# Optimization experiments

Hardware: AMD Instinct MI355X
Metric: run time of the kernel (lower is better)

## Reference

```python
import jax, jax.numpy as jnp
import numpy as np

B, T, P, D = 8, 2048, 4, 768

def setup_inputs() -> dict:
    key = jax.random.key(0)
    k1, k2, k3 = jax.random.split(key, 3)
    text_inputs = jax.random.normal(k1, (B, T, D), dtype=jnp.float32)
    sit_mask = jax.random.randint(k2, (B, T), 0, 2).astype(jnp.float32)
    proposition_matrix = jax.random.normal(k3, (B, T, P, D), dtype=jnp.float32)
    return {"text_inputs": text_inputs, "sit_mask": sit_mask, "proposition_matrix": proposition_matrix}

def reference(text_inputs, sit_mask, proposition_matrix):
    # D from proposition_matrix (matches text hidden dim), used for softmax scaling
    d = proposition_matrix.shape[-1]
    t = text_inputs.shape[1]
    # raw scores [B,T,T], scaled by 1/sqrt(D)
    scores = jnp.einsum('bid,bjd->bij', text_inputs, text_inputs) * (1.0 / jnp.sqrt(jnp.asarray(d, text_inputs.dtype)))
    # causal mask: strictly upper triangular -> -inf (tokens attend to self + past)
    causal = jnp.tril(jnp.ones((t, t), dtype=bool))  # [T,T]
    scores = jnp.where(causal[None, :, :], scores, -jnp.inf)
    weights = jax.nn.softmax(scores, axis=2)
    # padding mask via outer product of sit_mask; zero AFTER softmax (no renorm), as in original
    pad = (sit_mask[:, :, None] * sit_mask[:, None, :]) != 0  # [B,T,T]
    weights = jnp.where(pad, weights, jnp.zeros((), weights.dtype))
    out = jnp.einsum('bij,bjd->bid', weights, text_inputs)  # [B,T,D]
    # concat_self_hidden=True
    out = jnp.concatenate([out, text_inputs], axis=-1)  # [B,T,2D]
    return out
```

## Files before the change

kernel.cpp:

```cpp
#include <hip/hip_runtime.h>
#include <math.h>

constexpr int kT = 2048;
constexpr int kD = 768;

typedef __attribute__((ext_vector_type(8))) short short8;
typedef __attribute__((ext_vector_type(4))) float f32x4;
typedef __attribute__((ext_vector_type(16))) float f32x16;

#define FB(f) __builtin_bit_cast(unsigned, (f))
__device__ __forceinline__ unsigned pk_hi16(unsigned hi, unsigned lo) {
  return __builtin_amdgcn_perm(hi, lo, 0x07060302);
}
__device__ __forceinline__ unsigned pk_lo16(unsigned hi, unsigned lo) {
  return __builtin_amdgcn_perm(hi, lo, 0x05040100);
}

__device__ __forceinline__ void lds_barrier() {
  asm volatile("" ::: "memory");
  __builtin_amdgcn_s_waitcnt(0xC07F);
  __builtin_amdgcn_s_barrier();
  asm volatile("" ::: "memory");
}

__global__ __launch_bounds__(256, 2) void attn_mfma3(
    const float* __restrict__ x, const float* __restrict__ mask,
    float* __restrict__ out)
{
  const int tid = threadIdx.x;
  const int w = tid >> 6, l = tid & 63;
  const int l15 = l & 15, q4 = l >> 4;
  const int l31 = l & 31, h2 = l >> 5;

  const int bid = (int)blockIdx.x;
  const int b  = bid & 7;
  const int i0 = (63 - (bid >> 3)) << 5;

  const float* xb = x + (size_t)b * kT * kD;
  const float* mrow = mask + (size_t)b * kT;

  __shared__ unsigned short xK[16][776];
  __shared__ unsigned short VTb[192 * 64];
  __shared__ float sPart[4][16][36];
  __shared__ unsigned short Pm[32][16];
  __shared__ float corrS[32];
  __shared__ float invlS[32];

  short8 qf[2][6];
#pragma unroll
  for (int mt = 0; mt < 2; ++mt) {
    const int row = i0 + 16 * mt + l15;
#pragma unroll
    for (int s = 0; s < 6; ++s) {
      const float* p = xb + (size_t)row * kD + 192 * w + 32 * s + 8 * q4;
      float4 f0 = *(const float4*)p;
      float4 f1 = *(const float4*)(p + 4);
      uint4 u;
      u.x = pk_hi16(FB(f0.y), FB(f0.x));
      u.y = pk_hi16(FB(f0.w), FB(f0.z));
      u.z = pk_hi16(FB(f1.y), FB(f1.x));
      u.w = pk_hi16(FB(f1.w), FB(f1.z));
      qf[mt][s] = __builtin_bit_cast(short8, u);
    }
  }

  f32x16 o[6];
#pragma unroll
  for (int nt = 0; nt < 6; ++nt)
#pragma unroll
    for (int e = 0; e < 16; ++e) o[nt][e] = 0.0f;

  float mrun = -INFINITY, lrun = 0.0f;
  const float scale = 0.036084391824351615f;
  const int nTiles = i0 / 16 + 2;

  const int q = tid & 7, sr = tid >> 3;
  const int jA = (q >> 1) + 8 * (q & 1);
  const int irow = i0 + sr;

  const int D0 = 48 * w + (l31 >> 2);
  const int vtb_off0 = D0 * 64 + (((l31 & 3) ^ (D0 & 3)) << 4)
                     + ((8 * h2) ^ (8 * ((l31 >> 4) & 1)));

  float4 pf[3][4];
#pragma unroll
  for (int it = 0; it < 3; ++it)
#pragma unroll
    for (int jj = 0; jj < 4; ++jj)
      pf[it][jj] = *(const float4*)(xb + (size_t)(q4 + 4 * jj) * kD
                                    + 4 * (l15 + 16 * it + 48 * w));

  for (int t = 0; t < nTiles; ++t) {
    const int j0 = t * 16;
    const float mskA = mrow[j0 + jA];
    const float mskB = mrow[j0 + jA + 4];

    lds_barrier();

#pragma unroll
    for (int it = 0; it < 3; ++it) {
      const int d4 = l15 + 16 * it + 48 * w;
      unsigned lo[4], hi[4];
#pragma unroll
      for (int jj = 0; jj < 4; ++jj) {
        lo[jj] = pk_hi16(FB(pf[it][jj].y), FB(pf[it][jj].x));
        hi[jj] = pk_hi16(FB(pf[it][jj].w), FB(pf[it][jj].z));
      }
#pragma unroll
      for (int jj = 0; jj < 4; ++jj) {
        uint2 v; v.x = lo[jj]; v.y = hi[jj];
        *(uint2*)&xK[q4 + 4 * jj][4 * d4] = v;
      }
      const int D = d4;
      const int jb = (4 * q4) ^ (8 * ((D >> 2) & 1));
      const int base = D * 64 + jb;
      uint2 v;
      v.x = pk_lo16(lo[1], lo[0]); v.y = pk_lo16(lo[3], lo[2]);
      *(uint2*)&VTb[base + (((0 ^ (D & 3))) << 4)] = v;
      v.x = pk_hi16(lo[1], lo[0]); v.y = pk_hi16(lo[3], lo[2]);
      *(uint2*)&VTb[base + (((1 ^ (D & 3))) << 4)] = v;
      v.x = pk_lo16(hi[1], hi[0]); v.y = pk_lo16(hi[3], hi[2]);
      *(uint2*)&VTb[base + (((2 ^ (D & 3))) << 4)] = v;
      v.x = pk_hi16(hi[1], hi[0]); v.y = pk_hi16(hi[3], hi[2]);
      *(uint2*)&VTb[base + (((3 ^ (D & 3))) << 4)] = v;
    }

    if (t + 1 < nTiles) {
      const int jn = j0 + 16;
#pragma unroll
      for (int it = 0; it < 3; ++it)
#pragma unroll
        for (int jj = 0; jj < 4; ++jj)
          pf[it][jj] = *(const float4*)(xb + (size_t)(jn + q4 + 4 * jj) * kD
                                        + 4 * (l15 + 16 * it + 48 * w));
    }
    lds_barrier();

    {
      f32x4 sf0, sf1;
#pragma unroll
      for (int e = 0; e < 4; ++e) { sf0[e] = 0.f; sf1[e] = 0.f; }
#pragma unroll
      for (int s = 0; s < 6; ++s) {
        short8 kb = *(const short8*)&xK[l15][192 * w + 32 * s + 8 * q4];
        sf0 = __builtin_amdgcn_mfma_f32_16x16x32_bf16(qf[0][s], kb, sf0, 0, 0, 0);
        sf1 = __builtin_amdgcn_mfma_f32_16x16x32_bf16(qf[1][s], kb, sf1, 0, 0, 0);
      }
      *(f32x4*)&sPart[w][l15][4 * q4]      = sf0;
      *(f32x4*)&sPart[w][l15][16 + 4 * q4] = sf1;
    }
    lds_barrier();

    {
      float s0 = 0.f, s1 = 0.f;
#pragma unroll
      for (int ww = 0; ww < 4; ++ww) {
        s0 += sPart[ww][jA][sr];
        s1 += sPart[ww][jA + 4][sr];
      }
      const int ja = j0 + jA, jb_ = j0 + jA + 4;
      float a0 = (ja  <= irow) ? s0 * scale : -INFINITY;
      float a1 = (jb_ <= irow) ? s1 * scale : -INFINITY;
      float loc = fmaxf(a0, a1);
      loc = fmaxf(loc, __shfl_xor(loc, 1, 64));
      loc = fmaxf(loc, __shfl_xor(loc, 2, 64));
      loc = fmaxf(loc, __shfl_xor(loc, 4, 64));
      const float mn = fmaxf(mrun, loc);
      const float corr = __expf(mrun - mn);
      const float p0 = __expf(a0 - mn);
      const float p1 = __expf(a1 - mn);
      float rs = p0 + p1;
      rs += __shfl_xor(rs, 1, 64);
      rs += __shfl_xor(rs, 2, 64);
      rs += __shfl_xor(rs, 4, 64);
      lrun = lrun * corr + rs;
      mrun = mn;
      const float w0 = (mskA != 0.f) ? p0 : 0.f;
      const float w1 = (mskB != 0.f) ? p1 : 0.f;
      *(unsigned*)&Pm[sr][2 * q] = pk_hi16(FB(w1), FB(w0));
      if (q == 0) corrS[sr] = corr;
    }
    lds_barrier();

    {
      float cr[16];
#pragma unroll
      for (int e4 = 0; e4 < 4; ++e4) {
        f32x4 qd = *(const f32x4*)&corrS[8 * e4 + 4 * h2];
#pragma unroll
        for (int ee = 0; ee < 4; ++ee) cr[4 * e4 + ee] = qd[ee];
      }
#pragma unroll
      for (int nt = 0; nt < 6; ++nt)
#pragma unroll
        for (int e = 0; e < 16; ++e) o[nt][e] *= cr[e];
      short8 pa = *(const short8*)&Pm[l31][8 * h2];
#pragma unroll
      for (int nt = 0; nt < 6; ++nt) {
        short8 vb = *(const short8*)&VTb[vtb_off0 + 512 * nt];
        o[nt] = __builtin_amdgcn_mfma_f32_32x32x16_bf16(pa, vb, o[nt], 0, 0, 0);
      }
    }
  }

  if (q == 0) invlS[sr] = (mrow[irow] != 0.f) ? 1.0f / lrun : 0.0f;
  lds_barrier();
  {
    float il[16];
#pragma unroll
    for (int e4 = 0; e4 < 4; ++e4) {
      f32x4 qd = *(const f32x4*)&invlS[8 * e4 + 4 * h2];
#pragma unroll
      for (int ee = 0; ee < 4; ++ee) il[4 * e4 + ee] = qd[ee];
    }
    float* ob = out + (size_t)(b * kT + i0) * (2 * kD);
#pragma unroll
    for (int nt = 0; nt < 6; ++nt) {
      const int col = 192 * w + 32 * nt + l31;
#pragma unroll
      for (int e = 0; e < 16; ++e) {
        const int row = (e & 3) + 8 * (e >> 2) + 4 * h2;
        ob[(size_t)row * (2 * kD) + col] = o[nt][e] * il[e];
      }
    }
#pragma unroll
    for (int pass = 0; pass < 2; ++pass) {
      const int rr = (tid >> 4) + 16 * pass;
      const float* srcr = xb + (size_t)(i0 + rr) * kD;
      float* dstr = ob + (size_t)rr * (2 * kD) + kD;
#pragma unroll
      for (int it = 0; it < 12; ++it) {
        const int d4 = (tid & 15) + 16 * it;
        *(float4*)(dstr + 4 * d4) = *(const float4*)(srcr + 4 * d4);
      }
    }
  }
}

extern "C" void kernel_launch(void* const* d_in, const int* in_sizes, int n_in,
                              void* d_out, int out_size, void* d_ws, size_t ws_size,
                              hipStream_t stream) {
  const float* x    = (const float*)d_in[0];
  const float* mask = (const float*)d_in[1];
  float* out = (float*)d_out;
  attn_mfma3<<<dim3(512), dim3(256), 0, stream>>>(x, mask, out);
}
```

Measured before the change: 486.7 us.

## Precompute bf16 K and transposed V tiles, stream them via global_load_lds

Adds a prep kernel that converts x to bf16 once, writing both a swizzled row-major K layout and a transposed V layout into workspace. The attention kernel then stages K and V tiles straight into LDS with async global_load_lds, double-buffering the score, P and correction buffers so fewer barriers are needed. The mask row is loaded into LDS, and query-block order is reshuffled to balance causal work. This removes the repeated per-block fp32 loading and conversion, at the cost of an extra launch, workspace traffic and hand-tuned vmcnt waits that must be exactly right.

```diff
diff --git a/kernel.cpp b/kernel.cpp
--- a/kernel.cpp
+++ b/kernel.cpp
@@ -3,6 +3,8 @@
 
 constexpr int kT = 2048;
 constexpr int kD = 768;
+constexpr int kTileShorts = 16 * kD;
+constexpr int kTilesPerBatch = kT / 16;
 
 typedef __attribute__((ext_vector_type(8))) short short8;
 typedef __attribute__((ext_vector_type(4))) float f32x4;
@@ -23,8 +25,60 @@
   asm volatile("" ::: "memory");
 }
 
-__global__ __launch_bounds__(256, 2) void attn_mfma3(
+__device__ __forceinline__ void gload_lds16(const void* g, void* l) {
+  __builtin_amdgcn_global_load_lds(
+      (const __attribute__((address_space(1))) unsigned int*)g,
+      (__attribute__((address_space(3))) unsigned int*)l, 16, 0, 0);
+}
+
+__global__ __launch_bounds__(256) void prep_bf16(
+    const float* __restrict__ x,
+    unsigned short* __restrict__ xbf, unsigned short* __restrict__ xvt)
+{
+  const int tid = threadIdx.x;
+  const int w = tid >> 6, l = tid & 63;
+  const int l15 = l & 15, q4 = l >> 4;
+  const int bt = (int)blockIdx.x;
+  const float* xb = x + (size_t)bt * 16 * kD;
+  unsigned short* ob = xbf + (size_t)bt * kTileShorts;
+  unsigned short* ov = xvt + (size_t)bt * kTileShorts;
+
+#pragma unroll
+  for (int it = 0; it < 3; ++it) {
+    const int dq = l15 + 16 * it + 48 * w;
+    unsigned lo[4], hi[4];
+#pragma unroll
+    for (int jj = 0; jj < 4; ++jj) {
+      const float4 f = *(const float4*)(xb + (size_t)(q4 + 4 * jj) * kD + 4 * dq);
+      lo[jj] = pk_hi16(FB(f.y), FB(f.x));
+      hi[jj] = pk_hi16(FB(f.w), FB(f.z));
+    }
+    const int dp = 4 * (l15 + 16 * it);
+    const int g = dp >> 3, e0 = dp & 7;
+#pragma unroll
+    for (int jj = 0; jj < 4; ++jj) {
+      const int j = q4 + 4 * jj;
+      uint2 v; v.x = lo[jj]; v.y = hi[jj];
+      *(uint2*)&ob[w * 3072 + j * 192 + ((g ^ (j & 7)) << 3) + e0] = v;
+    }
+    const int jb = (4 * q4) ^ (8 * ((dq >> 2) & 1));
+    const int base = dq * 64 + jb;
+    uint2 v;
+    v.x = pk_lo16(lo[1], lo[0]); v.y = pk_lo16(lo[3], lo[2]);
+    *(uint2*)&ov[base + ((0 ^ (dq & 3)) << 4)] = v;
+    v.x = pk_hi16(lo[1], lo[0]); v.y = pk_hi16(lo[3], lo[2]);
+    *(uint2*)&ov[base + ((1 ^ (dq & 3)) << 4)] = v;
+    v.x = pk_lo16(hi[1], hi[0]); v.y = pk_lo16(hi[3], hi[2]);
+    *(uint2*)&ov[base + ((2 ^ (dq & 3)) << 4)] = v;
+    v.x = pk_hi16(hi[1], hi[0]); v.y = pk_hi16(hi[3], hi[2]);
+    *(uint2*)&ov[base + ((3 ^ (dq & 3)) << 4)] = v;
+  }
+}
+
+__global__ __launch_bounds__(256, 2) void attn_mfma4(
     const float* __restrict__ x, const float* __restrict__ mask,
+    const unsigned short* __restrict__ xbf,
+    const unsigned short* __restrict__ xvt,
     float* __restrict__ out)
 {
   const int tid = threadIdx.x;
@@ -33,35 +87,39 @@
   const int l31 = l & 31, h2 = l >> 5;
 
   const int bid = (int)blockIdx.x;
-  const int b  = bid & 7;
-  const int i0 = (63 - (bid >> 3)) << 5;
+  const int b = bid & 7;
+  const int s = bid >> 3;
+  const int qq = (s < 32) ? (63 - s) : (s - 32);
+  const int i0 = qq << 5;
 
   const float* xb = x + (size_t)b * kT * kD;
   const float* mrow = mask + (size_t)b * kT;
-
-  __shared__ unsigned short xK[16][776];
-  __shared__ unsigned short VTb[192 * 64];
-  __shared__ float sPart[4][16][36];
-  __shared__ unsigned short Pm[32][16];
-  __shared__ float corrS[32];
+  const unsigned short* xbfB = xbf + (size_t)b * kTilesPerBatch * kTileShorts;
+  const unsigned short* xvtB = xvt + (size_t)b * kTilesPerBatch * kTileShorts;
+
+  __shared__ unsigned short xKc[12288];
+  __shared__ unsigned short VTb[12288];
+  __shared__ float sPart[2][4][16][36];
+  __shared__ unsigned short Pm[2][32][16];
+  __shared__ float corrS[2][32];
   __shared__ float invlS[32];
+  __shared__ float msk[kT];
+
+  {
+    const char* msrc = (const char*)mrow + 2048 * w;
+    char* mdst = (char*)&msk[512 * w];
+    gload_lds16(msrc + 16 * l, mdst);
+    gload_lds16(msrc + 1024 + 16 * l, mdst + 1024);
+  }
 
   short8 qf[2][6];
 #pragma unroll
   for (int mt = 0; mt < 2; ++mt) {
-    const int row = i0 + 16 * mt + l15;
-#pragma unroll
-    for (int s = 0; s < 6; ++s) {
-      const float* p = xb + (size_t)row * kD + 192 * w + 32 * s + 8 * q4;
-      float4 f0 = *(const float4*)p;
-      float4 f1 = *(const float4*)(p + 4);
-      uint4 u;
-      u.x = pk_hi16(FB(f0.y), FB(f0.x));
-      u.y = pk_hi16(FB(f0.w), FB(f0.z));
-      u.z = pk_hi16(FB(f1.y), FB(f1.x));
-      u.w = pk_hi16(FB(f1.w), FB(f1.z));
-      qf[mt][s] = __builtin_bit_cast(short8, u);
-    }
+    const int tq = (i0 >> 4) + mt;
+    const unsigned short* tp = xbfB + (size_t)tq * kTileShorts + w * 3072 + l15 * 192;
+#pragma unroll
+    for (int s6 = 0; s6 < 6; ++s6)
+      qf[mt][s6] = *(const short8*)&tp[((4 * s6 + q4) ^ (l15 & 7)) << 3];
   }
 
   f32x16 o[6];
@@ -82,72 +140,48 @@
   const int vtb_off0 = D0 * 64 + (((l31 & 3) ^ (D0 & 3)) << 4)
                      + ((8 * h2) ^ (8 * ((l31 >> 4) & 1)));
 
-  float4 pf[3][4];
-#pragma unroll
-  for (int it = 0; it < 3; ++it)
-#pragma unroll
-    for (int jj = 0; jj < 4; ++jj)
-      pf[it][jj] = *(const float4*)(xb + (size_t)(q4 + 4 * jj) * kD
-                                    + 4 * (l15 + 16 * it + 48 * w));
+  auto stageK = [&](int t) {
+    const unsigned short* src = xbfB + (size_t)t * kTileShorts + w * 3072 + 8 * l;
+    unsigned short* dst = &xKc[w * 3072];
+#pragma unroll
+    for (int i = 0; i < 6; ++i) gload_lds16(src + 512 * i, dst + 512 * i);
+  };
+  auto stageV = [&](int t) {
+    const unsigned short* src = xvtB + (size_t)t * kTileShorts + w * 3072 + 8 * l;
+    unsigned short* dst = &VTb[w * 3072];
+#pragma unroll
+    for (int i = 0; i < 6; ++i) gload_lds16(src + 512 * i, dst + 512 * i);
+  };
+
+  stageK(0);
+  stageV(0);
+  asm volatile("s_waitcnt vmcnt(12)" ::: "memory");
+  lds_barrier();
 
   for (int t = 0; t < nTiles; ++t) {
-    const int j0 = t * 16;
-    const float mskA = mrow[j0 + jA];
-    const float mskB = mrow[j0 + jA + 4];
-
-    lds_barrier();
-
-#pragma unroll
-    for (int it = 0; it < 3; ++it) {
-      const int d4 = l15 + 16 * it + 48 * w;
-      unsigned lo[4], hi[4];
-#pragma unroll
-      for (int jj = 0; jj < 4; ++jj) {
-        lo[jj] = pk_hi16(FB(pf[it][jj].y), FB(pf[it][jj].x));
-        hi[jj] = pk_hi16(FB(pf[it][jj].w), FB(pf[it][jj].z));
-      }
-#pragma unroll
-      for (int jj = 0; jj < 4; ++jj) {
-        uint2 v; v.x = lo[jj]; v.y = hi[jj];
-        *(uint2*)&xK[q4 + 4 * jj][4 * d4] = v;
-      }
-      const int D = d4;
-      const int jb = (4 * q4) ^ (8 * ((D >> 2) & 1));
-      const int base = D * 64 + jb;
-      uint2 v;
-      v.x = pk_lo16(lo[1], lo[0]); v.y = pk_lo16(lo[3], lo[2]);
-      *(uint2*)&VTb[base + (((0 ^ (D & 3))) << 4)] = v;
-      v.x = pk_hi16(lo[1], lo[0]); v.y = pk_hi16(lo[3], lo[2]);
-      *(uint2*)&VTb[base + (((1 ^ (D & 3))) << 4)] = v;
-      v.x = pk_lo16(hi[1], hi[0]); v.y = pk_lo16(hi[3], hi[2]);
-      *(uint2*)&VTb[base + (((2 ^ (D & 3))) << 4)] = v;
-      v.x = pk_hi16(hi[1], hi[0]); v.y = pk_hi16(hi[3], hi[2]);
-      *(uint2*)&VTb[base + (((3 ^ (D & 3))) << 4)] = v;
-    }
-
-    if (t + 1 < nTiles) {
-      const int jn = j0 + 16;
-#pragma unroll
-      for (int it = 0; it < 3; ++it)
-#pragma unroll
-        for (int jj = 0; jj < 4; ++jj)
-          pf[it][jj] = *(const float4*)(xb + (size_t)(jn + q4 + 4 * jj) * kD
-                                        + 4 * (l15 + 16 * it + 48 * w));
-    }
-    lds_barrier();
+    const int par = t & 1;
+    const int j0 = t << 4;
+
+    asm volatile("s_waitcnt vmcnt(6)" ::: "memory");
 
     {
       f32x4 sf0, sf1;
 #pragma unroll
       for (int e = 0; e < 4; ++e) { sf0[e] = 0.f; sf1[e] = 0.f; }
-#pragma unroll
-      for (int s = 0; s < 6; ++s) {
-        short8 kb = *(const short8*)&xK[l15][192 * w + 32 * s + 8 * q4];
-        sf0 = __builtin_amdgcn_mfma_f32_16x16x32_bf16(qf[0][s], kb, sf0, 0, 0, 0);
-        sf1 = __builtin_amdgcn_mfma_f32_16x16x32_bf16(qf[1][s], kb, sf1, 0, 0, 0);
-      }
-      *(f32x4*)&sPart[w][l15][4 * q4]      = sf0;
-      *(f32x4*)&sPart[w][l15][16 + 4 * q4] = sf1;
+      const unsigned short* kbase = &xKc[w * 3072 + l15 * 192];
+#pragma unroll
+      for (int s6 = 0; s6 < 6; ++s6) {
+        short8 kb = *(const short8*)&kbase[((4 * s6 + q4) ^ (l15 & 7)) << 3];
+        sf0 = __builtin_amdgcn_mfma_f32_16x16x32_bf16(qf[0][s6], kb, sf0, 0, 0, 0);
+        sf1 = __builtin_amdgcn_mfma_f32_16x16x32_bf16(qf[1][s6], kb, sf1, 0, 0, 0);
+      }
+      *(f32x4*)&sPart[par][w][l15][4 * q4]      = sf0;
+      *(f32x4*)&sPart[par][w][l15][16 + 4 * q4] = sf1;
+    }
+
+    if (t + 1 < nTiles) {
+      asm volatile("s_waitcnt lgkmcnt(0)" ::: "memory");
+      stageK(t + 1);
     }
     lds_barrier();
 
@@ -155,9 +189,11 @@
       float s0 = 0.f, s1 = 0.f;
 #pragma unroll
       for (int ww = 0; ww < 4; ++ww) {
-        s0 += sPart[ww][jA][sr];
-        s1 += sPart[ww][jA + 4][sr];
-      }
+        s0 += sPart[par][ww][jA][sr];
+        s1 += sPart[par][ww][jA + 4][sr];
+      }
+      const float mskA = msk[j0 + jA];
+      const float mskB = msk[j0 + jA + 4];
       const int ja = j0 + jA, jb_ = j0 + jA + 4;
       float a0 = (ja  <= irow) ? s0 * scale : -INFINITY;
       float a1 = (jb_ <= irow) ? s1 * scale : -INFINITY;
@@ -177,16 +213,19 @@
       mrun = mn;
       const float w0 = (mskA != 0.f) ? p0 : 0.f;
       const float w1 = (mskB != 0.f) ? p1 : 0.f;
-      *(unsigned*)&Pm[sr][2 * q] = pk_hi16(FB(w1), FB(w0));
-      if (q == 0) corrS[sr] = corr;
+      *(unsigned*)&Pm[par][sr][2 * q] = pk_hi16(FB(w1), FB(w0));
+      if (q == 0) corrS[par][sr] = corr;
     }
     lds_barrier();
+
+    if (t + 1 < nTiles) { asm volatile("s_waitcnt vmcnt(6)" ::: "memory"); }
+    else                { asm volatile("s_waitcnt vmcnt(0)" ::: "memory"); }
 
     {
       float cr[16];
 #pragma unroll
       for (int e4 = 0; e4 < 4; ++e4) {
-        f32x4 qd = *(const f32x4*)&corrS[8 * e4 + 4 * h2];
+        f32x4 qd = *(const f32x4*)&corrS[par][8 * e4 + 4 * h2];
 #pragma unroll
         for (int ee = 0; ee < 4; ++ee) cr[4 * e4 + ee] = qd[ee];
       }
@@ -194,16 +233,21 @@
       for (int nt = 0; nt < 6; ++nt)
 #pragma unroll
         for (int e = 0; e < 16; ++e) o[nt][e] *= cr[e];
-      short8 pa = *(const short8*)&Pm[l31][8 * h2];
+      short8 pa = *(const short8*)&Pm[par][l31][8 * h2];
 #pragma unroll
       for (int nt = 0; nt < 6; ++nt) {
         short8 vb = *(const short8*)&VTb[vtb_off0 + 512 * nt];
         o[nt] = __builtin_amdgcn_mfma_f32_32x32x16_bf16(pa, vb, o[nt], 0, 0, 0);
       }
     }
-  }
-
-  if (q == 0) invlS[sr] = (mrow[irow] != 0.f) ? 1.0f / lrun : 0.0f;
+
+    if (t + 1 < nTiles) {
+      asm volatile("s_waitcnt lgkmcnt(0)" ::: "memory");
+      stageV(t + 1);
+    }
+  }
+
+  if (q == 0) invlS[sr] = (msk[irow] != 0.f) ? 1.0f / lrun : 0.0f;
   lds_barrier();
   {
     float il[16];
@@ -243,5 +287,8 @@
   const float* x    = (const float*)d_in[0];
   const float* mask = (const float*)d_in[1];
   float* out = (float*)d_out;
-  attn_mfma3<<<dim3(512), dim3(256), 0, stream>>>(x, mask, out);
-}
+  unsigned short* xbf = (unsigned short*)d_ws;
+  unsigned short* xvt = xbf + (size_t)8 * kTilesPerBatch * kTileShorts;
+  prep_bf16<<<dim3(8 * kTilesPerBatch), dim3(256), 0, stream>>>(x, xbf, xvt);
+  attn_mfma4<<<dim3(512), dim3(256), 0, stream>>>(x, mask, xbf, xvt, out);
+}
```

Result: faster. 462.4 us (-5.0%).
